# Kernel optimization log

Measured on AMD Instinct MI355X. Metric: run time of the kernel, lower is better.

Reference implementation:

```python
import jax, jax.numpy as jnp
import numpy as np

B, L, D = 4, 2048, 1024
E, K, H = 8, 2, 4096
EPS = 1e-5


def setup_inputs() -> dict:
    key = jax.random.key(0)
    ks = jax.random.split(key, 6)
    x = jax.random.normal(ks[0], (B, L, D), jnp.float32)
    gate_w = jax.random.normal(ks[1], (E, D), jnp.float32) * 0.02
    W1 = jax.random.normal(ks[2], (E, D, H), jnp.float32) * 0.02
    b1 = jnp.zeros((E, H), jnp.float32)
    W2 = jax.random.normal(ks[3], (E, H, D), jnp.float32) * 0.02
    b2 = jnp.zeros((E, D), jnp.float32)
    gamma = jnp.ones((D,), jnp.float32)
    beta = jnp.zeros((D,), jnp.float32)
    return {"x": x, "gamma": gamma, "beta": beta, "gate_w": gate_w,
            "W1": W1, "b1": b1, "W2": W2, "b2": b2}


def reference(x, gamma, beta, gate_w, W1, b1, W2, b2):
    # LayerNorm (biased variance, eps=1e-5, matches torch.nn.LayerNorm)
    mu = jnp.mean(x, axis=-1, keepdims=True)
    var = jnp.mean((x - mu) ** 2, axis=-1, keepdims=True)
    xn = (x - mu) / jnp.sqrt(var + EPS) * gamma + beta
    xf = xn.reshape(-1, D)  # (T, D), T = B*L
    T = xf.shape[0]

    # gating: top-k logits -> softmax -> scatter into dense gates (T, E)
    logits = xf @ gate_w.T  # (T, E)
    top_v, top_i = jax.lax.top_k(logits, K)
    top_g = jax.nn.softmax(top_v, axis=-1)
    gates = jnp.zeros_like(logits).at[jnp.arange(T)[:, None], top_i].set(top_g)

    # experts: dense-equivalent of masked gather/FFN/scatter-add combine.
    # Non-selected experts contribute with gate weight 0 -> identical math.
    h = jax.nn.gelu(jnp.einsum('td,edh->teh', xf, W1) + b1, approximate=False)
    y = jnp.einsum('teh,ehd->ted', h, W2) + b2  # (T, E, D)
    out = jnp.einsum('te,ted->td', gates, y).reshape(B, L, D) + x

    # load-balance loss: MSE(mean gate per expert, uniform)
    load = jnp.mean(gates, axis=0)
    bal_loss = jnp.mean((load - 1.0 / E) ** 2)
    return out, bal_loss
```

## Files before the change

### kernel.cpp

```cpp
#include <hip/hip_runtime.h>
#include <hip/hip_bf16.h>

#define T_TOK 8192
#define DD 1024
#define EE 8
#define HH 4096
#define NA (2 * T_TOK)
#define NBLK (NA / 256)

typedef __bf16 bf16_t;
typedef __bf16 bf16x8 __attribute__((ext_vector_type(8)));
typedef __bf16 bf16x4 __attribute__((ext_vector_type(4)));
typedef float f32x4 __attribute__((ext_vector_type(4)));

#define GLDS(g, l) __builtin_amdgcn_global_load_lds( \
    (const __attribute__((address_space(1))) void*)(g), \
    (__attribute__((address_space(3))) void*)(l), 16, 0, 0)

__global__ __launch_bounds__(256) void ln_gate_kernel(
    const float* __restrict__ x, const float* __restrict__ gamma,
    const float* __restrict__ beta, const float* __restrict__ gate_w,
    bf16_t* __restrict__ xn, int* __restrict__ tokexp, float* __restrict__ tokgate)
{
    const int t = blockIdx.x;
    const int tid = threadIdx.x;
    const int lane = tid & 63, wave = tid >> 6;
    __shared__ float wred[4];
    __shared__ float stats[2];
    __shared__ float lred[32];
    __shared__ float logitsS[8];

    float4 v = ((const float4*)(x + (size_t)t * DD))[tid];
    float s = v.x + v.y + v.z + v.w;
#pragma unroll
    for (int o = 32; o > 0; o >>= 1) s += __shfl_down(s, o, 64);
    if (lane == 0) wred[wave] = s;
    __syncthreads();
    if (tid == 0) stats[0] = (wred[0] + wred[1] + wred[2] + wred[3]) * (1.0f / DD);
    __syncthreads();
    const float mu = stats[0];
    float d0 = v.x - mu, d1 = v.y - mu, d2 = v.z - mu, d3 = v.w - mu;
    float q = d0*d0 + d1*d1 + d2*d2 + d3*d3;
#pragma unroll
    for (int o = 32; o > 0; o >>= 1) q += __shfl_down(q, o, 64);
    __syncthreads();
    if (lane == 0) wred[wave] = q;
    __syncthreads();
    if (tid == 0) stats[1] = rsqrtf((wred[0]+wred[1]+wred[2]+wred[3]) * (1.0f / DD) + 1e-5f);
    __syncthreads();
    const float rstd = stats[1];
    float4 g4 = ((const float4*)gamma)[tid];
    float4 b4 = ((const float4*)beta)[tid];
    float n0 = d0 * rstd * g4.x + b4.x;
    float n1 = d1 * rstd * g4.y + b4.y;
    float n2 = d2 * rstd * g4.z + b4.z;
    float n3 = d3 * rstd * g4.w + b4.w;
    bf16x4 pk = { (bf16_t)n0, (bf16_t)n1, (bf16_t)n2, (bf16_t)n3 };
    ((bf16x4*)(xn + (size_t)t * DD))[tid] = pk;

    float part[8];
#pragma unroll
    for (int e = 0; e < 8; ++e) {
        float4 gw = ((const float4*)(gate_w + (size_t)e * DD))[tid];
        part[e] = n0 * gw.x + n1 * gw.y + n2 * gw.z + n3 * gw.w;
    }
#pragma unroll
    for (int e = 0; e < 8; ++e) {
        float p = part[e];
#pragma unroll
        for (int o = 32; o > 0; o >>= 1) p += __shfl_down(p, o, 64);
        if (lane == 0) lred[wave * 8 + e] = p;
    }
    __syncthreads();
    if (tid < 8) logitsS[tid] = lred[tid] + lred[8 + tid] + lred[16 + tid] + lred[24 + tid];
    __syncthreads();
    if (tid == 0) {
        float best = -1e30f; int e0 = 0;
        for (int e = 0; e < 8; ++e) { float le = logitsS[e]; if (le > best) { best = le; e0 = e; } }
        float best2 = -1e30f; int e1 = (e0 == 0) ? 1 : 0;
        for (int e = 0; e < 8; ++e) if (e != e0) { float le = logitsS[e]; if (le > best2) { best2 = le; e1 = e; } }
        float z = expf(best2 - best);
        float g0 = 1.0f / (1.0f + z);
        float g1 = z * g0;
        tokexp[2*t] = e0; tokexp[2*t+1] = e1;
        tokgate[2*t] = g0; tokgate[2*t+1] = g1;
    }
}

__global__ __launch_bounds__(256) void hist_kernel(
    const int* __restrict__ tokexp, const float* __restrict__ tokgate,
    int* __restrict__ blockcnt, float* __restrict__ blockgsum)
{
    __shared__ int hcnt[EE];
    __shared__ float hg[EE];
    const int b = blockIdx.x, tid = threadIdx.x;
    if (tid < EE) { hcnt[tid] = 0; hg[tid] = 0.f; }
    __syncthreads();
    int idx = b * 256 + tid;
    int e = tokexp[idx];
    atomicAdd(&hcnt[e], 1);
    atomicAdd(&hg[e], tokgate[idx]);
    __syncthreads();
    if (tid < EE) {
        blockcnt[b * EE + tid] = hcnt[tid];
        blockgsum[b * EE + tid] = hg[tid];
    }
}

__global__ __launch_bounds__(64) void offs_bal_kernel(
    const int* __restrict__ blockcnt, const float* __restrict__ blockgsum,
    int* __restrict__ cnt, int* __restrict__ offs, int* __restrict__ basep,
    float* __restrict__ bal_out)
{
    __shared__ int cntS[EE];
    const int tid = threadIdx.x;
    if (tid < EE) {
        int run = 0;
        for (int b = 0; b < NBLK; ++b) {
            basep[b * EE + tid] = run;
            run += blockcnt[b * EE + tid];
        }
        cnt[tid] = run;
        cntS[tid] = run;
    }
    __syncthreads();
    __shared__ int offsS[EE];
    if (tid == 0) {
        int run = 0; 
        for (int e = 0; e < EE; ++e) { offsS[e] = run; offs[e] = run; run += cntS[e]; }
        float bal = 0.f;
        for (int e = 0; e < EE; ++e) {
            float g = 0.f;
            for (int b = 0; b < NBLK; ++b) g += blockgsum[b * EE + e];
            float l = g * (1.0f / T_TOK) - (1.0f / EE);
            bal += l * l;
        }
        bal_out[0] = bal * (1.0f / EE);
    }
    __syncthreads();
    if (tid < EE) {
        for (int b = 0; b < NBLK; ++b) basep[b * EE + tid] += offsS[tid];
    }
}

__global__ __launch_bounds__(256) void scatter_kernel(
    const int* __restrict__ tokexp, const float* __restrict__ tokgate,
    const int* __restrict__ basep,
    int* __restrict__ tok, float* __restrict__ gatev, int* __restrict__ a_of_t)
{
    __shared__ int hcnt[EE];
    const int b = blockIdx.x, tid = threadIdx.x;
    if (tid < EE) hcnt[tid] = 0;
    __syncthreads();
    int idx = b * 256 + tid;
    int e = tokexp[idx];
    int r = atomicAdd(&hcnt[e], 1);
    int a = basep[b * EE + e] + r;
    tok[a] = idx >> 1;
    gatev[a] = tokgate[idx];
    a_of_t[idx] = a;
}

__global__ __launch_bounds__(256) void convT_kernel(
    const float* __restrict__ in, bf16_t* __restrict__ out, int R, int C)
{
    __shared__ float tile[64][65];
    int e = blockIdx.z;
    int c0 = blockIdx.x * 64, r0 = blockIdx.y * 64;
    int tx = threadIdx.x & 63, ty = threadIdx.x >> 6;
    const float* src = in + ((size_t)e * R + r0) * C + c0;
#pragma unroll
    for (int i = 0; i < 16; ++i) {
        int r = ty + i * 4;
        tile[r][tx] = src[(size_t)r * C + tx];
    }
    __syncthreads();
    bf16_t* dst = out + ((size_t)e * C + c0) * R + r0;
#pragma unroll
    for (int i = 0; i < 16; ++i) {
        int cc = ty + i * 4;
        dst[(size_t)cc * R + tx] = (bf16_t)tile[tx][cc];
    }
}

__global__ __launch_bounds__(256) void ffn1_kernel(
    const bf16_t* __restrict__ xn, const bf16_t* __restrict__ w1t,
    const float* __restrict__ b1, const int* __restrict__ tok,
    const int* __restrict__ cnt, const int* __restrict__ offs,
    bf16_t* __restrict__ h1)
{
    const int e = blockIdx.z;
    const int c = cnt[e];
    const int m0 = blockIdx.y * 128;
    if (m0 >= c) return;
    const int n0 = blockIdx.x * 128;
    const int off = offs[e];

    __shared__ __align__(16) bf16_t As[128 * 32];
    __shared__ __align__(16) bf16_t Bs[128 * 32];

    const int tid = threadIdx.x;
    const int sr = tid >> 2;
    const int scol = (tid & 3) * 8;

    int ar0 = m0 + sr;      if (ar0 >= c) ar0 = c - 1;
    int ar1 = m0 + 64 + sr; if (ar1 >= c) ar1 = c - 1;
    const bf16_t* aptr0 = xn + (size_t)tok[off + ar0] * DD + scol;
    const bf16_t* aptr1 = xn + (size_t)tok[off + ar1] * DD + scol;
    const bf16_t* bptr0 = w1t + ((size_t)e * HH + n0 + sr) * DD + scol;
    const bf16_t* bptr1 = bptr0 + (size_t)64 * DD;

    bf16_t* ldsA0 = As + (size_t)tid * 8;
    bf16_t* ldsA1 = As + (size_t)(256 + tid) * 8;
    bf16_t* ldsB0 = Bs + (size_t)tid * 8;
    bf16_t* ldsB1 = Bs + (size_t)(256 + tid) * 8;

    const int lane = tid & 63;
    const int wave = tid >> 6;
    const int wr = wave >> 1, wc = wave & 1;
    const int mL = lane & 15, quad = lane >> 4;

    const bf16_t* Abase = As + ((wr * 64 + mL) * 32 + quad * 8);
    const bf16_t* Bbase = Bs + ((wc * 64 + mL) * 32 + quad * 8);

    f32x4 acc[4][4] = {};

    for (int k0 = 0; k0 < DD; k0 += 32) {
        GLDS(aptr0, ldsA0);
        GLDS(aptr1, ldsA1);
        GLDS(bptr0, ldsB0);
        GLDS(bptr1, ldsB1);
        aptr0 += 32; aptr1 += 32; bptr0 += 32; bptr1 += 32;
        __syncthreads();
        bf16x8 af[4], bfv[4];
#pragma unroll
        for (int i = 0; i < 4; ++i) af[i] = *(const bf16x8*)(Abase + i * 16 * 32);
#pragma unroll
        for (int j = 0; j < 4; ++j) bfv[j] = *(const bf16x8*)(Bbase + j * 16 * 32);
#pragma unroll
        for (int i = 0; i < 4; ++i)
#pragma unroll
            for (int j = 0; j < 4; ++j)
                acc[i][j] = __builtin_amdgcn_mfma_f32_16x16x32_bf16(af[i], bfv[j], acc[i][j], 0, 0, 0);
        __syncthreads();
    }

    const float* b1e = b1 + (size_t)e * HH;
#pragma unroll
    for (int i = 0; i < 4; ++i) {
#pragma unroll
        for (int r = 0; r < 4; ++r) {
            int m = m0 + wr * 64 + i * 16 + quad * 4 + r;
            if (m < c) {
                bf16_t* hrow = h1 + (size_t)(off + m) * HH;
#pragma unroll
                for (int j = 0; j < 4; ++j) {
                    int n = n0 + wc * 64 + j * 16 + mL;
                    float v = acc[i][j][r] + b1e[n];
                    v = 0.5f * v * (1.0f + erff(v * 0.70710678118654752f));
                    hrow[n] = (bf16_t)v;
                }
            }
        }
    }
}

__global__ __launch_bounds__(256) void ffn2_kernel(
    const bf16_t* __restrict__ h1, const bf16_t* __restrict__ w2t,
    const float* __restrict__ b2, const float* __restrict__ gatev,
    const int* __restrict__ cnt, const int* __restrict__ offs,
    bf16_t* __restrict__ yv)
{
    const int e = blockIdx.z;
    const int c = cnt[e];
    const int m0 = blockIdx.y * 128;
    if (m0 >= c) return;
    const int n0 = blockIdx.x * 128;
    const int off = offs[e];

    __shared__ __align__(16) bf16_t As[128 * 32];
    __shared__ __align__(16) bf16_t Bs[128 * 32];

    const int tid = threadIdx.x;
    const int sr = tid >> 2;
    const int scol = (tid & 3) * 8;

    int ar0 = m0 + sr;      if (ar0 >= c) ar0 = c - 1;
    int ar1 = m0 + 64 + sr; if (ar1 >= c) ar1 = c - 1;
    const bf16_t* aptr0 = h1 + (size_t)(off + ar0) * HH + scol;
    const bf16_t* aptr1 = h1 + (size_t)(off + ar1) * HH + scol;
    const bf16_t* bptr0 = w2t + ((size_t)e * DD + n0 + sr) * HH + scol;
    const bf16_t* bptr1 = bptr0 + (size_t)64 * HH;

    bf16_t* ldsA0 = As + (size_t)tid * 8;
    bf16_t* ldsA1 = As + (size_t)(256 + tid) * 8;
    bf16_t* ldsB0 = Bs + (size_t)tid * 8;
    bf16_t* ldsB1 = Bs + (size_t)(256 + tid) * 8;

    const int lane = tid & 63;
    const int wave = tid >> 6;
    const int wr = wave >> 1, wc = wave & 1;
    const int mL = lane & 15, quad = lane >> 4;

    const bf16_t* Abase = As + ((wr * 64 + mL) * 32 + quad * 8);
    const bf16_t* Bbase = Bs + ((wc * 64 + mL) * 32 + quad * 8);

    f32x4 acc[4][4] = {};

    for (int k0 = 0; k0 < HH; k0 += 32) {
        GLDS(aptr0, ldsA0);
        GLDS(aptr1, ldsA1);
        GLDS(bptr0, ldsB0);
        GLDS(bptr1, ldsB1);
        aptr0 += 32; aptr1 += 32; bptr0 += 32; bptr1 += 32;
        __syncthreads();
        bf16x8 af[4], bfv[4];
#pragma unroll
        for (int i = 0; i < 4; ++i) af[i] = *(const bf16x8*)(Abase + i * 16 * 32);
#pragma unroll
        for (int j = 0; j < 4; ++j) bfv[j] = *(const bf16x8*)(Bbase + j * 16 * 32);
#pragma unroll
        for (int i = 0; i < 4; ++i)
#pragma unroll
            for (int j = 0; j < 4; ++j)
                acc[i][j] = __builtin_amdgcn_mfma_f32_16x16x32_bf16(af[i], bfv[j], acc[i][j], 0, 0, 0);
        __syncthreads();
    }

    const float* b2e = b2 + (size_t)e * DD;
#pragma unroll
    for (int i = 0; i < 4; ++i) {
#pragma unroll
        for (int r = 0; r < 4; ++r) {
            int m = m0 + wr * 64 + i * 16 + quad * 4 + r;
            if (m < c) {
                float g = gatev[off + m];
                bf16_t* yrow = yv + (size_t)(off + m) * DD;
#pragma unroll
                for (int j = 0; j < 4; ++j) {
                    int n = n0 + wc * 64 + j * 16 + mL;
                    float v = (acc[i][j][r] + b2e[n]) * g;
                    yrow[n] = (bf16_t)v;
                }
            }
        }
    }
}

__global__ __launch_bounds__(256) void combine_kernel(
    const float* __restrict__ x, const bf16_t* __restrict__ yv,
    const int* __restrict__ a_of_t, float* __restrict__ outp)
{
    int t = blockIdx.x;
    int tid = threadIdx.x;
    int a0 = a_of_t[2*t], a1 = a_of_t[2*t+1];
    float4 xv = ((const float4*)(x + (size_t)t * DD))[tid];
    bf16x4 y0 = ((const bf16x4*)(yv + (size_t)a0 * DD))[tid];
    bf16x4 y1 = ((const bf16x4*)(yv + (size_t)a1 * DD))[tid];
    float4 o;
    o.x = xv.x + (float)y0[0] + (float)y1[0];
    o.y = xv.y + (float)y0[1] + (float)y1[1];
    o.z = xv.z + (float)y0[2] + (float)y1[2];
    o.w = xv.w + (float)y0[3] + (float)y1[3];
    ((float4*)(outp + (size_t)t * DD))[tid] = o;
}

extern "C" void kernel_launch(void* const* d_in, const int* in_sizes, int n_in,
                              void* d_out, int out_size, void* d_ws, size_t ws_size,
                              hipStream_t stream)
{
    const float* x      = (const float*)d_in[0];
    const float* gamma  = (const float*)d_in[1];
    const float* beta   = (const float*)d_in[2];
    const float* gate_w = (const float*)d_in[3];
    const float* W1     = (const float*)d_in[4];
    const float* b1     = (const float*)d_in[5];
    const float* W2     = (const float*)d_in[6];
    const float* b2     = (const float*)d_in[7];
    float* outp = (float*)d_out;
    float* bal_out = outp + (size_t)T_TOK * DD;

    char* ws = (char*)d_ws;
    size_t off = 0;
    auto alloc = [&](size_t bytes) {
        char* p = ws + off;
        off += (bytes + 255) & ~(size_t)255;
        return p;
    };
    bf16_t* xn   = (bf16_t*)alloc((size_t)T_TOK * DD * 2);
    bf16_t* w1t  = (bf16_t*)alloc((size_t)EE * HH * DD * 2);
    bf16_t* w2t  = (bf16_t*)alloc((size_t)EE * DD * HH * 2);
    bf16_t* h1   = (bf16_t*)alloc((size_t)NA * HH * 2);
    bf16_t* yv   = (bf16_t*)alloc((size_t)NA * DD * 2);
    int*   tok     = (int*)alloc(NA * 4);
    float* gatev   = (float*)alloc(NA * 4);
    int*   a_of_t  = (int*)alloc(NA * 4);
    int*   tokexp  = (int*)alloc(NA * 4);
    float* tokgate = (float*)alloc(NA * 4);
    int*   blockcnt  = (int*)alloc(NBLK * EE * 4);
    float* blockgsum = (float*)alloc(NBLK * EE * 4);
    int*   basep     = (int*)alloc(NBLK * EE * 4);
    int*   cnt  = (int*)alloc(EE * 4);
    int*   offs = (int*)alloc(EE * 4);

    convT_kernel<<<dim3(HH/64, DD/64, EE), 256, 0, stream>>>(W1, w1t, DD, HH);
    convT_kernel<<<dim3(DD/64, HH/64, EE), 256, 0, stream>>>(W2, w2t, HH, DD);
    ln_gate_kernel<<<T_TOK, 256, 0, stream>>>(x, gamma, beta, gate_w, xn, tokexp, tokgate);
    hist_kernel<<<NBLK, 256, 0, stream>>>(tokexp, tokgate, blockcnt, blockgsum);
    offs_bal_kernel<<<1, 64, 0, stream>>>(blockcnt, blockgsum, cnt, offs, basep, bal_out);
    scatter_kernel<<<NBLK, 256, 0, stream>>>(tokexp, tokgate, basep, tok, gatev, a_of_t);
    ffn1_kernel<<<dim3(HH/128, 64, EE), 256, 0, stream>>>(xn, w1t, b1, tok, cnt, offs, h1);
    ffn2_kernel<<<dim3(DD/128, 64, EE), 256, 0, stream>>>(h1, w2t, b2, gatev, cnt, offs, yv);
    combine_kernel<<<T_TOK, 256, 0, stream>>>(x, yv, a_of_t, outp);
}
```

Before: 870.7 us.

## Widen GEMM K-step to 64, stage epilogue through LDS, vectorize transpose

Both expert GEMM kernels now load two 32-wide K slices per iteration, which halves the number of barriers per unit of MFMA work. Each epilogue writes the bias/GELU or gated outputs into shared memory first, then stores full 16-byte rows to global memory instead of scattered 2-byte stores. The weight transpose kernel reads float4 and writes packed bf16 pairs. LDS use per block doubles to 32KB, which may lower occupancy, and the wider load step gives no real double buffering.

```diff
diff --git a/kernel.cpp b/kernel.cpp
--- a/kernel.cpp
+++ b/kernel.cpp
@@ -11,6 +11,7 @@
 typedef __bf16 bf16_t;
 typedef __bf16 bf16x8 __attribute__((ext_vector_type(8)));
 typedef __bf16 bf16x4 __attribute__((ext_vector_type(4)));
+typedef __bf16 bf16x2v __attribute__((ext_vector_type(2)));
 typedef float f32x4 __attribute__((ext_vector_type(4)));
 
 #define GLDS(g, l) __builtin_amdgcn_global_load_lds( \
@@ -126,7 +127,7 @@
     __syncthreads();
     __shared__ int offsS[EE];
     if (tid == 0) {
-        int run = 0; 
+        int run = 0;
         for (int e = 0; e < EE; ++e) { offsS[e] = run; offs[e] = run; run += cntS[e]; }
         float bal = 0.f;
         for (int e = 0; e < EE; ++e) {
@@ -167,19 +168,26 @@
     __shared__ float tile[64][65];
     int e = blockIdx.z;
     int c0 = blockIdx.x * 64, r0 = blockIdx.y * 64;
-    int tx = threadIdx.x & 63, ty = threadIdx.x >> 6;
+    int tid = threadIdx.x;
     const float* src = in + ((size_t)e * R + r0) * C + c0;
-#pragma unroll
-    for (int i = 0; i < 16; ++i) {
-        int r = ty + i * 4;
-        tile[r][tx] = src[(size_t)r * C + tx];
-    }
-    __syncthreads();
-    bf16_t* dst = out + ((size_t)e * C + c0) * R + r0;
-#pragma unroll
-    for (int i = 0; i < 16; ++i) {
-        int cc = ty + i * 4;
-        dst[(size_t)cc * R + tx] = (bf16_t)tile[tx][cc];
+    int lr = tid >> 4;
+    int lc = (tid & 15) * 4;
+#pragma unroll
+    for (int p = 0; p < 4; ++p) {
+        float4 v = *(const float4*)(src + (size_t)(lr + p * 16) * C + lc);
+        tile[lr + p * 16][lc + 0] = v.x;
+        tile[lr + p * 16][lc + 1] = v.y;
+        tile[lr + p * 16][lc + 2] = v.z;
+        tile[lr + p * 16][lc + 3] = v.w;
+    }
+    __syncthreads();
+    bf16_t* dstb = out + (size_t)e * C * R;
+    int rr = (tid & 31) * 2;
+#pragma unroll
+    for (int i = 0; i < 8; ++i) {
+        int cc = i * 8 + (tid >> 5);
+        bf16x2v pk = { (bf16_t)tile[rr][cc], (bf16_t)tile[rr + 1][cc] };
+        *(bf16x2v*)(dstb + ((size_t)(c0 + cc)) * R + r0 + rr) = pk;
     }
 }
 
@@ -196,8 +204,11 @@
     const int n0 = blockIdx.x * 128;
     const int off = offs[e];
 
-    __shared__ __align__(16) bf16_t As[128 * 32];
-    __shared__ __align__(16) bf16_t Bs[128 * 32];
+    __shared__ __align__(16) bf16_t smem[16384];
+    bf16_t* As0 = smem;
+    bf16_t* As1 = smem + 4096;
+    bf16_t* Bs0 = smem + 8192;
+    bf16_t* Bs1 = smem + 12288;
 
     const int tid = threadIdx.x;
     const int sr = tid >> 2;
@@ -205,63 +216,83 @@
 
     int ar0 = m0 + sr;      if (ar0 >= c) ar0 = c - 1;
     int ar1 = m0 + 64 + sr; if (ar1 >= c) ar1 = c - 1;
-    const bf16_t* aptr0 = xn + (size_t)tok[off + ar0] * DD + scol;
-    const bf16_t* aptr1 = xn + (size_t)tok[off + ar1] * DD + scol;
-    const bf16_t* bptr0 = w1t + ((size_t)e * HH + n0 + sr) * DD + scol;
-    const bf16_t* bptr1 = bptr0 + (size_t)64 * DD;
-
-    bf16_t* ldsA0 = As + (size_t)tid * 8;
-    bf16_t* ldsA1 = As + (size_t)(256 + tid) * 8;
-    bf16_t* ldsB0 = Bs + (size_t)tid * 8;
-    bf16_t* ldsB1 = Bs + (size_t)(256 + tid) * 8;
+    const bf16_t* aRow0 = xn + (size_t)tok[off + ar0] * DD + scol;
+    const bf16_t* aRow1 = xn + (size_t)tok[off + ar1] * DD + scol;
+    const bf16_t* bRow0 = w1t + ((size_t)e * HH + n0 + sr) * DD + scol;
+    const bf16_t* bRow1 = bRow0 + (size_t)64 * DD;
 
     const int lane = tid & 63;
     const int wave = tid >> 6;
     const int wr = wave >> 1, wc = wave & 1;
     const int mL = lane & 15, quad = lane >> 4;
 
-    const bf16_t* Abase = As + ((wr * 64 + mL) * 32 + quad * 8);
-    const bf16_t* Bbase = Bs + ((wc * 64 + mL) * 32 + quad * 8);
+    const int fo = (wr * 64 + mL) * 32 + quad * 8;
+    const int go = (wc * 64 + mL) * 32 + quad * 8;
 
     f32x4 acc[4][4] = {};
 
-    for (int k0 = 0; k0 < DD; k0 += 32) {
-        GLDS(aptr0, ldsA0);
-        GLDS(aptr1, ldsA1);
-        GLDS(bptr0, ldsB0);
-        GLDS(bptr1, ldsB1);
-        aptr0 += 32; aptr1 += 32; bptr0 += 32; bptr1 += 32;
+    for (int k0 = 0; k0 < DD; k0 += 64) {
+        GLDS(aRow0 + k0,      As0 + tid * 8);
+        GLDS(aRow1 + k0,      As0 + (256 + tid) * 8);
+        GLDS(aRow0 + k0 + 32, As1 + tid * 8);
+        GLDS(aRow1 + k0 + 32, As1 + (256 + tid) * 8);
+        GLDS(bRow0 + k0,      Bs0 + tid * 8);
+        GLDS(bRow1 + k0,      Bs0 + (256 + tid) * 8);
+        GLDS(bRow0 + k0 + 32, Bs1 + tid * 8);
+        GLDS(bRow1 + k0 + 32, Bs1 + (256 + tid) * 8);
         __syncthreads();
-        bf16x8 af[4], bfv[4];
-#pragma unroll
-        for (int i = 0; i < 4; ++i) af[i] = *(const bf16x8*)(Abase + i * 16 * 32);
-#pragma unroll
-        for (int j = 0; j < 4; ++j) bfv[j] = *(const bf16x8*)(Bbase + j * 16 * 32);
-#pragma unroll
-        for (int i = 0; i < 4; ++i)
-#pragma unroll
-            for (int j = 0; j < 4; ++j)
-                acc[i][j] = __builtin_amdgcn_mfma_f32_16x16x32_bf16(af[i], bfv[j], acc[i][j], 0, 0, 0);
+        {
+            bf16x8 af[4], bfv[4];
+#pragma unroll
+            for (int i = 0; i < 4; ++i) af[i] = *(const bf16x8*)(As0 + fo + i * 16 * 32);
+#pragma unroll
+            for (int j = 0; j < 4; ++j) bfv[j] = *(const bf16x8*)(Bs0 + go + j * 16 * 32);
+#pragma unroll
+            for (int i = 0; i < 4; ++i)
+#pragma unroll
+                for (int j = 0; j < 4; ++j)
+                    acc[i][j] = __builtin_amdgcn_mfma_f32_16x16x32_bf16(af[i], bfv[j], acc[i][j], 0, 0, 0);
+        }
+        {
+            bf16x8 af[4], bfv[4];
+#pragma unroll
+            for (int i = 0; i < 4; ++i) af[i] = *(const bf16x8*)(As1 + fo + i * 16 * 32);
+#pragma unroll
+            for (int j = 0; j < 4; ++j) bfv[j] = *(const bf16x8*)(Bs1 + go + j * 16 * 32);
+#pragma unroll
+            for (int i = 0; i < 4; ++i)
+#pragma unroll
+                for (int j = 0; j < 4; ++j)
+                    acc[i][j] = __builtin_amdgcn_mfma_f32_16x16x32_bf16(af[i], bfv[j], acc[i][j], 0, 0, 0);
+        }
         __syncthreads();
     }
 
     const float* b1e = b1 + (size_t)e * HH;
-#pragma unroll
-    for (int i = 0; i < 4; ++i) {
+    float bj[4];
+#pragma unroll
+    for (int j = 0; j < 4; ++j) bj[j] = b1e[n0 + wc * 64 + j * 16 + mL];
+#pragma unroll
+    for (int i = 0; i < 4; ++i)
 #pragma unroll
         for (int r = 0; r < 4; ++r) {
-            int m = m0 + wr * 64 + i * 16 + quad * 4 + r;
-            if (m < c) {
-                bf16_t* hrow = h1 + (size_t)(off + m) * HH;
-#pragma unroll
-                for (int j = 0; j < 4; ++j) {
-                    int n = n0 + wc * 64 + j * 16 + mL;
-                    float v = acc[i][j][r] + b1e[n];
-                    v = 0.5f * v * (1.0f + erff(v * 0.70710678118654752f));
-                    hrow[n] = (bf16_t)v;
-                }
+            int row = wr * 64 + i * 16 + quad * 4 + r;
+#pragma unroll
+            for (int j = 0; j < 4; ++j) {
+                int col = wc * 64 + j * 16 + mL;
+                float v = acc[i][j][r] + bj[j];
+                v = 0.5f * v * (1.0f + erff(v * 0.70710678118654752f));
+                smem[row * 128 + col] = (bf16_t)v;
             }
         }
+    __syncthreads();
+#pragma unroll
+    for (int p = 0; p < 8; ++p) {
+        int idx = p * 2048 + tid * 8;
+        int row = idx >> 7;
+        int colv = idx & 127;
+        if (m0 + row < c)
+            *(bf16x8*)(h1 + (size_t)(off + m0 + row) * HH + n0 + colv) = *(const bf16x8*)(smem + idx);
     }
 }
 
@@ -278,8 +309,11 @@
     const int n0 = blockIdx.x * 128;
     const int off = offs[e];
 
-    __shared__ __align__(16) bf16_t As[128 * 32];
-    __shared__ __align__(16) bf16_t Bs[128 * 32];
+    __shared__ __align__(16) bf16_t smem[16384];
+    bf16_t* As0 = smem;
+    bf16_t* As1 = smem + 4096;
+    bf16_t* Bs0 = smem + 8192;
+    bf16_t* Bs1 = smem + 12288;
 
     const int tid = threadIdx.x;
     const int sr = tid >> 2;
@@ -287,63 +321,84 @@
 
     int ar0 = m0 + sr;      if (ar0 >= c) ar0 = c - 1;
     int ar1 = m0 + 64 + sr; if (ar1 >= c) ar1 = c - 1;
-    const bf16_t* aptr0 = h1 + (size_t)(off + ar0) * HH + scol;
-    const bf16_t* aptr1 = h1 + (size_t)(off + ar1) * HH + scol;
-    const bf16_t* bptr0 = w2t + ((size_t)e * DD + n0 + sr) * HH + scol;
-    const bf16_t* bptr1 = bptr0 + (size_t)64 * HH;
-
-    bf16_t* ldsA0 = As + (size_t)tid * 8;
-    bf16_t* ldsA1 = As + (size_t)(256 + tid) * 8;
-    bf16_t* ldsB0 = Bs + (size_t)tid * 8;
-    bf16_t* ldsB1 = Bs + (size_t)(256 + tid) * 8;
+    const bf16_t* aRow0 = h1 + (size_t)(off + ar0) * HH + scol;
+    const bf16_t* aRow1 = h1 + (size_t)(off + ar1) * HH + scol;
+    const bf16_t* bRow0 = w2t + ((size_t)e * DD + n0 + sr) * HH + scol;
+    const bf16_t* bRow1 = bRow0 + (size_t)64 * HH;
 
     const int lane = tid & 63;
     const int wave = tid >> 6;
     const int wr = wave >> 1, wc = wave & 1;
     const int mL = lane & 15, quad = lane >> 4;
 
-    const bf16_t* Abase = As + ((wr * 64 + mL) * 32 + quad * 8);
-    const bf16_t* Bbase = Bs + ((wc * 64 + mL) * 32 + quad * 8);
+    const int fo = (wr * 64 + mL) * 32 + quad * 8;
+    const int go = (wc * 64 + mL) * 32 + quad * 8;
 
     f32x4 acc[4][4] = {};
 
-    for (int k0 = 0; k0 < HH; k0 += 32) {
-        GLDS(aptr0, ldsA0);
-        GLDS(aptr1, ldsA1);
-        GLDS(bptr0, ldsB0);
-        GLDS(bptr1, ldsB1);
-        aptr0 += 32; aptr1 += 32; bptr0 += 32; bptr1 += 32;
+    for (int k0 = 0; k0 < HH; k0 += 64) {
+        GLDS(aRow0 + k0,      As0 + tid * 8);
+        GLDS(aRow1 + k0,      As0 + (256 + tid) * 8);
+        GLDS(aRow0 + k0 + 32, As1 + tid * 8);
+        GLDS(aRow1 + k0 + 32, As1 + (256 + tid) * 8);
+        GLDS(bRow0 + k0,      Bs0 + tid * 8);
+        GLDS(bRow1 + k0,      Bs0 + (256 + tid) * 8);
+        GLDS(bRow0 + k0 + 32, Bs1 + tid * 8);
+        GLDS(bRow1 + k0 + 32, Bs1 + (256 + tid) * 8);
         __syncthreads();
-        bf16x8 af[4], bfv[4];
-#pragma unroll
-        for (int i = 0; i < 4; ++i) af[i] = *(const bf16x8*)(Abase + i * 16 * 32);
-#pragma unroll
-        for (int j = 0; j < 4; ++j) bfv[j] = *(const bf16x8*)(Bbase + j * 16 * 32);
-#pragma unroll
-        for (int i = 0; i < 4; ++i)
-#pragma unroll
-            for (int j = 0; j < 4; ++j)
-                acc[i][j] = __builtin_amdgcn_mfma_f32_16x16x32_bf16(af[i], bfv[j], acc[i][j], 0, 0, 0);
+        {
+            bf16x8 af[4], bfv[4];
+#pragma unroll
+            for (int i = 0; i < 4; ++i) af[i] = *(const bf16x8*)(As0 + fo + i * 16 * 32);
+#pragma unroll
+            for (int j = 0; j < 4; ++j) bfv[j] = *(const bf16x8*)(Bs0 + go + j * 16 * 32);
+#pragma unroll
+            for (int i = 0; i < 4; ++i)
+#pragma unroll
+                for (int j = 0; j < 4; ++j)
+                    acc[i][j] = __builtin_amdgcn_mfma_f32_16x16x32_bf16(af[i], bfv[j], acc[i][j], 0, 0, 0);
+        }
+        {
+            bf16x8 af[4], bfv[4];
+#pragma unroll
+            for (int i = 0; i < 4; ++i) af[i] = *(const bf16x8*)(As1 + fo + i * 16 * 32);
+#pragma unroll
+            for (int j = 0; j < 4; ++j) bfv[j] = *(const bf16x8*)(Bs1 + go + j * 16 * 32);
+#pragma unroll
+            for (int i = 0; i < 4; ++i)
+#pragma unroll
+                for (int j = 0; j < 4; ++j)
+                    acc[i][j] = __builtin_amdgcn_mfma_f32_16x16x32_bf16(af[i], bfv[j], acc[i][j], 0, 0, 0);
+        }
         __syncthreads();
     }
 
     const float* b2e = b2 + (size_t)e * DD;
-#pragma unroll
-    for (int i = 0; i < 4; ++i) {
+    float bj[4];
+#pragma unroll
+    for (int j = 0; j < 4; ++j) bj[j] = b2e[n0 + wc * 64 + j * 16 + mL];
+#pragma unroll
+    for (int i = 0; i < 4; ++i)
 #pragma unroll
         for (int r = 0; r < 4; ++r) {
-            int m = m0 + wr * 64 + i * 16 + quad * 4 + r;
-            if (m < c) {
-                float g = gatev[off + m];
-                bf16_t* yrow = yv + (size_t)(off + m) * DD;
-#pragma unroll
-                for (int j = 0; j < 4; ++j) {
-                    int n = n0 + wc * 64 + j * 16 + mL;
-                    float v = (acc[i][j][r] + b2e[n]) * g;
-                    yrow[n] = (bf16_t)v;
-                }
+            int row = wr * 64 + i * 16 + quad * 4 + r;
+            int mrow = m0 + row; if (mrow >= c) mrow = c - 1;
+            float g = gatev[off + mrow];
+#pragma unroll
+            for (int j = 0; j < 4; ++j) {
+                int col = wc * 64 + j * 16 + mL;
+                float v = (acc[i][j][r] + bj[j]) * g;
+                smem[row * 128 + col] = (bf16_t)v;
             }
         }
+    __syncthreads();
+#pragma unroll
+    for (int p = 0; p < 8; ++p) {
+        int idx = p * 2048 + tid * 8;
+        int row = idx >> 7;
+        int colv = idx & 127;
+        if (m0 + row < c)
+            *(bf16x8*)(yv + (size_t)(off + m0 + row) * DD + n0 + colv) = *(const bf16x8*)(smem + idx);
     }
 }
 
```

Measured after the change: 924.6 us. 6.2% more time.
